# Performance work log

Measured on AMD Instinct MI355X. Metric: run time of the kernel, lower is better.

Reference implementation:

```python
import jax, jax.numpy as jnp
import numpy as np

T = S = 1024
B = 8
HID = 1024
H = 16
D = HID // H          # head_size = 64
RELK = 16             # max relative position (clip window)
NEG = -1e9


def setup_inputs() -> dict:
    key = jax.random.key(0)
    ks = jax.random.split(key, 12)
    inv = 1.0 / np.sqrt(HID)
    inp = {
        'q': jax.random.normal(ks[0], (T, B, HID), jnp.float32),
        'k': jax.random.normal(ks[1], (S, B, HID), jnp.float32),
        'v': jax.random.normal(ks[2], (S, B, HID), jnp.float32),
        # additive float mask (B,T,S): causal, masked positions = -1e9
        'mask': jnp.broadcast_to(jnp.triu(jnp.full((T, S), NEG, jnp.float32), k=1), (B, T, S)),
        'Wq': jax.random.normal(ks[3], (HID, HID), jnp.float32) * inv,
        'bq': jnp.zeros((HID,), jnp.float32),
        'Wk': jax.random.normal(ks[4], (HID, HID), jnp.float32) * inv,
        'bk': jnp.zeros((HID,), jnp.float32),
        'Wv': jax.random.normal(ks[5], (HID, HID), jnp.float32) * inv,
        'bv': jnp.zeros((HID,), jnp.float32),
        'Wo': jax.random.normal(ks[6], (HID, HID), jnp.float32) * inv,
        'bo': jnp.zeros((HID,), jnp.float32),
        'rel_k_table': jax.random.normal(ks[7], (2 * RELK + 1, D), jnp.float32) * 0.02,
        'rel_v_table': jax.random.normal(ks[8], (2 * RELK + 1, D), jnp.float32) * 0.02,
    }
    return inp


def _rel_index(t, s):
    # clipped relative position index (t, s) -> [0, 2*RELK]
    return jnp.clip(jnp.arange(s)[None, :] - jnp.arange(t)[:, None], -RELK, RELK) + RELK


def reference(q, k, v, mask, Wq, bq, Wk, bk, Wv, bv, Wo, bo, rel_k_table, rel_v_table):
    t, b, _ = q.shape
    scaling = D ** -0.5
    # projections; torch Linear: x @ W^T + b, here weights stored (in,out)
    qh = ((q @ Wq + bq) * scaling).reshape(t, b * H, D).transpose(1, 0, 2)  # (BH,T,D)
    kh = (k @ Wk + bk).reshape(-1, b * H, D).transpose(1, 0, 2)            # (BH,S,D)
    vh = (v @ Wv + bv).reshape(-1, b * H, D).transpose(1, 0, 2)            # (BH,S,D)
    s = kh.shape[1]

    score = jnp.einsum('ntd,nsd->nts', qh, kh)                 # (BH,T,S)
    idx = _rel_index(t, s)
    rel_k = rel_k_table[idx]                                   # (T,S,D)
    score = score + jnp.einsum('ntd,tsd->nts', qh, rel_k)      # relative-pos bias on scores

    score = (score.reshape(b, H, t, s) + mask[:, None]).reshape(b * H, t, s)
    attn = jax.nn.softmax(score, axis=-1)                      # dropout=0 (eval)

    o = jnp.einsum('nts,nsd->ntd', attn, vh)                   # (BH,T,D)
    rel_v = rel_v_table[idx]                                   # (T,S,D)
    o = o + jnp.einsum('nts,tsd->ntd', attn, rel_v)            # relative-pos bias on values

    o = o.transpose(1, 0, 2).reshape(t, b, H * D)              # (T,B,hidden)
    return o @ Wo + bo
```

## Files before the change

### kernel.cpp

```cpp
#include <hip/hip_runtime.h>

typedef unsigned short u16;
typedef __bf16 bf16x8 __attribute__((ext_vector_type(8)));
typedef __bf16 bf16x4v __attribute__((ext_vector_type(4)));
typedef short s16x4 __attribute__((ext_vector_type(4)));
typedef unsigned short u16x8 __attribute__((ext_vector_type(8)));
typedef unsigned short u16x4 __attribute__((ext_vector_type(4)));
typedef float f32x4 __attribute__((ext_vector_type(4)));


__device__ __forceinline__ u16 f2bf(float f) {
  return __builtin_bit_cast(u16, (__bf16)f);
}
__device__ __forceinline__ u16x8 pack_trunc8(float4 a, float4 b) {
  u16x8 t;
  t[0] = (u16)(__float_as_uint(a.x) >> 16); t[1] = (u16)(__float_as_uint(a.y) >> 16);
  t[2] = (u16)(__float_as_uint(a.z) >> 16); t[3] = (u16)(__float_as_uint(a.w) >> 16);
  t[4] = (u16)(__float_as_uint(b.x) >> 16); t[5] = (u16)(__float_as_uint(b.y) >> 16);
  t[6] = (u16)(__float_as_uint(b.z) >> 16); t[7] = (u16)(__float_as_uint(b.w) >> 16);
  return t;
}
__device__ __forceinline__ void barrier_lgkm() {
  __asm__ volatile("s_waitcnt lgkmcnt(0)\ns_barrier" ::: "memory");
}
typedef const __attribute__((address_space(1))) void* gas_ptr;
typedef __attribute__((address_space(3))) void* las_ptr;
__device__ __forceinline__ void load_lds16(const void* g, void* l) {
  __builtin_amdgcn_global_load_lds((gas_ptr)g, (las_ptr)l, 16, 0, 0);
}
__device__ __forceinline__ f32x4 mfma16(u16x4 a, u16x4 b, f32x4 c) {
#if __has_builtin(__builtin_amdgcn_mfma_f32_16x16x16_bf16)
  return __builtin_amdgcn_mfma_f32_16x16x16_bf16(
      __builtin_bit_cast(bf16x4v, a), __builtin_bit_cast(bf16x4v, b), c, 0, 0, 0);
#elif __has_builtin(__builtin_amdgcn_mfma_f32_16x16x16bf16_1k)
  return __builtin_amdgcn_mfma_f32_16x16x16bf16_1k(
      __builtin_bit_cast(s16x4, a), __builtin_bit_cast(s16x4, b), c, 0, 0, 0);
#else
  f32x4 d;
  __asm__ volatile("v_mfma_f32_16x16x16_bf16 %0, %1, %2, %3"
                   : "=v"(d) : "v"(a), "v"(b), "v"(c));
  return d;
#endif
}

__device__ __forceinline__ void transpose_body(const float* in, u16* out) {
  __shared__ u16 tile[64][65];
  const int r0 = blockIdx.y * 64, c0 = blockIdx.x * 64;
  const int tid = threadIdx.x;
  const int tr = tid >> 4, tc4 = (tid & 15) * 4;
#pragma unroll
  for (int p = 0; p < 4; ++p) {
    int r = tr + p * 16;
    float4 vv = *(const float4*)&in[(size_t)(r0 + r) * 1024 + c0 + tc4];
    tile[r][tc4 + 0] = f2bf(vv.x); tile[r][tc4 + 1] = f2bf(vv.y);
    tile[r][tc4 + 2] = f2bf(vv.z); tile[r][tc4 + 3] = f2bf(vv.w);
  }
  __syncthreads();
#pragma unroll
  for (int p = 0; p < 4; ++p) {
    int rr = tr + p * 16;
    ushort4 ov;
    ov.x = tile[tc4 + 0][rr]; ov.y = tile[tc4 + 1][rr];
    ov.z = tile[tc4 + 2][rr]; ov.w = tile[tc4 + 3][rr];
    *(ushort4*)&out[(size_t)(c0 + rr) * 1024 + r0 + tc4] = ov;
  }
}
__global__ __launch_bounds__(256) void transpose_cvt3_kernel(
    const float* w0, const float* w1, const float* w2,
    u16* o0, u16* o1, u16* o2)
{
  const float* in = blockIdx.z == 0 ? w0 : (blockIdx.z == 1 ? w1 : w2);
  u16* out = blockIdx.z == 0 ? o0 : (blockIdx.z == 1 ? o1 : o2);
  transpose_body(in, out);
}
__global__ __launch_bounds__(256) void transpose_cvt_kernel(
    const float* in, u16* out) { transpose_body(in, out); }

__global__ __launch_bounds__(256) void cvt3_kernel(
    const float* __restrict__ a, const float* __restrict__ b,
    const float* __restrict__ c,
    u16* __restrict__ oa, u16* __restrict__ ob, u16* __restrict__ oc)
{
  const float* in = blockIdx.z == 0 ? a : (blockIdx.z == 1 ? b : c);
  u16* out = blockIdx.z == 0 ? oa : (blockIdx.z == 1 ? ob : oc);
  const int n8 = (8192 * 1024) / 8;
  for (int i = blockIdx.x * 256 + threadIdx.x; i < n8; i += gridDim.x * 256) {
    float4 x = ((const float4*)in)[i * 2];
    float4 y = ((const float4*)in)[i * 2 + 1];
    *(u16x8*)&out[(size_t)i * 8] = pack_trunc8(x, y);
  }
}

struct GemmArgs {
  const u16* A; const u16* BT; const float* bias; void* out;
  float scale; int mode;
};

__global__ __launch_bounds__(256, 3) void gemm_lds_kernel(GemmArgs g0, GemmArgs g1)
{
  __shared__ __align__(16) u16 smem[24576];
  const GemmArgs g = blockIdx.z ? g1 : g0;
  const u16* __restrict__ A = g.A;
  const u16* __restrict__ BT = g.BT;
  const int tid = threadIdx.x;
  const int wave = tid >> 6, lane = tid & 63;
  const int quad = lane >> 4, l16 = lane & 15;
  const int wave_m = wave >> 1, wave_n = wave & 1;
  const int m0 = blockIdx.x * 128, n0 = blockIdx.y * 128;

  const int crow = tid >> 2;
  const int cq = (((tid & 3) ^ ((tid >> 3) & 3))) * 8;
  const int qswr = (quad ^ ((l16 >> 1) & 3)) * 8;

  f32x4 acc[4][4] = {};

  auto STAGE = [&](int bo, int kb) {
    const size_t ka = (size_t)kb * 32 + cq;
    load_lds16(&A [(size_t)(m0 + crow)      * 1024 + ka], &smem[bo + tid * 8]);
    load_lds16(&A [(size_t)(m0 + 64 + crow) * 1024 + ka], &smem[bo + 2048 + tid * 8]);
    load_lds16(&BT[(size_t)(n0 + crow)      * 1024 + ka], &smem[bo + 4096 + tid * 8]);
    load_lds16(&BT[(size_t)(n0 + 64 + crow) * 1024 + ka], &smem[bo + 6144 + tid * 8]);
  };

  int b0 = 0, b1 = 8192, b2 = 16384;
  STAGE(b0, 0);
  STAGE(b1, 1);
  for (int kb = 0; kb < 32; ++kb) {
    if (kb < 31)
      __asm__ volatile("s_waitcnt vmcnt(4) lgkmcnt(0)\ns_barrier" ::: "memory");
    else
      __asm__ volatile("s_waitcnt vmcnt(0) lgkmcnt(0)\ns_barrier" ::: "memory");
    if (kb + 2 < 32) STAGE(b2, kb + 2);
    const u16* As = &smem[b0];
    const u16* Bs = &smem[b0 + 4096];
    bf16x8 af[4], bfr[4];
#pragma unroll
    for (int mt = 0; mt < 4; ++mt)
      af[mt] = *(const bf16x8*)&As[(wave_m * 64 + mt * 16 + l16) * 32 + qswr];
#pragma unroll
    for (int nt = 0; nt < 4; ++nt)
      bfr[nt] = *(const bf16x8*)&Bs[(wave_n * 64 + nt * 16 + l16) * 32 + qswr];
#pragma unroll
    for (int mt = 0; mt < 4; ++mt)
#pragma unroll
      for (int nt = 0; nt < 4; ++nt)
        acc[mt][nt] = __builtin_amdgcn_mfma_f32_16x16x32_bf16(af[mt], bfr[nt], acc[mt][nt], 0, 0, 0);
    int t = b0; b0 = b1; b1 = b2; b2 = t;
  }

  const float scale = g.scale;
  if (g.mode == 0) {
#pragma unroll
    for (int mt = 0; mt < 4; ++mt)
#pragma unroll
      for (int nt = 0; nt < 4; ++nt) {
        int nn = n0 + wave_n * 64 + nt * 16 + l16;
        float bval = g.bias[nn];
#pragma unroll
        for (int reg = 0; reg < 4; ++reg) {
          int mm = m0 + wave_m * 64 + mt * 16 + quad * 4 + reg;
          ((float*)g.out)[(size_t)mm * 1024 + nn] = (acc[mt][nt][reg] + bval) * scale;
        }
      }
  } else {
    __syncthreads();
    u16* Cs = smem;
#pragma unroll
    for (int mt = 0; mt < 4; ++mt)
#pragma unroll
      for (int nt = 0; nt < 4; ++nt) {
        int nnl = wave_n * 64 + nt * 16 + l16;
        float bval = g.bias[n0 + nnl];
#pragma unroll
        for (int reg = 0; reg < 4; ++reg) {
          int mml = wave_m * 64 + mt * 16 + quad * 4 + reg;
          Cs[mml * 136 + nnl] = f2bf((acc[mt][nt][reg] + bval) * scale);
        }
      }
    __syncthreads();
    u16* out = (u16*)g.out;
    if (g.mode == 1) {
      int row = tid >> 1, half = tid & 1;
      int mm = m0 + row;
      int tt = mm >> 3, bbv = mm & 7;
      int hh = (n0 >> 6) + half;
      u16* dst = &out[(((size_t)(bbv * 16 + hh)) * 1024 + tt) * 64];
#pragma unroll
      for (int i = 0; i < 8; ++i)
        *(u16x8*)&dst[i * 8] = *(const u16x8*)&Cs[row * 136 + half * 64 + i * 8];
    } else {
      int t0 = m0 >> 3;
#pragma unroll
      for (int rr = 0; rr < 4; ++rr) {
        int rid = tid * 4 + rr;
        int nnv = rid >> 3, bbv = rid & 7;
        int hh = (n0 + nnv) >> 6, dd = (n0 + nnv) & 63;
        u16* dst = &out[(((size_t)(bbv * 16 + hh)) * 64 + dd) * 1024 + t0];
        u16x8 w0, w1;
#pragma unroll
        for (int t = 0; t < 8; ++t) w0[t] = Cs[(t * 8 + bbv) * 136 + nnv];
#pragma unroll
        for (int t = 0; t < 8; ++t) w1[t] = Cs[((t + 8) * 8 + bbv) * 136 + nnv];
        *(u16x8*)&dst[0] = w0;
        *(u16x8*)&dst[8] = w1;
      }
    }
  }
}

__global__ __launch_bounds__(256, 4) void attn_kernel(
    const u16* __restrict__ qh, const u16* __restrict__ kh,
    const u16* __restrict__ vt, const float* __restrict__ relk,
    const float* __restrict__ relv, u16* __restrict__ octx)
{
  const int n = blockIdx.x;
  const int q0 = (15 - blockIdx.y) * 64;
  const int tid = threadIdx.x;
  const int wave = tid >> 6, lane = tid & 63;
  const int quad = lane >> 4, l16 = lane & 15;
  const int rowi = wave * 16 + l16;
  const int trow = q0 + rowi;
  const float LOG2E = 1.442695040888963f;

  __shared__ __align__(16) u16 Ks[64 * 72];
  __shared__ __align__(16) u16 Vs[64 * 72];
  __shared__ float qrelS[64 * 17];
  __shared__ float wvS[17 * 64];
  __shared__ float relvS[17 * 64];

  const int diag = q0 >> 6;
  const int ntiles = diag + 1;

  bf16x8 qf[2];
#pragma unroll
  for (int kc = 0; kc < 2; ++kc)
    qf[kc] = *(const bf16x8*)&qh[((size_t)n * 1024 + trow) * 64 + kc * 32 + quad * 8];

  const u16* __restrict__ khn = kh + (size_t)n * 1024 * 64;
  const u16* __restrict__ vtn = vt + (size_t)n * 64 * 1024;

  u16x8 kA[2], vA[2], kB[2], vB[2];
  auto LOADT = [&](int s0, u16x8 (&kr)[2], u16x8 (&vr)[2]) {
#pragma unroll
    for (int j = 0; j < 2; ++j) {
      int c = j * 256 + tid;
      kr[j] = *(const u16x8*)&khn[(size_t)(s0 + (c >> 3)) * 64 + (c & 7) * 8];
      vr[j] = *(const u16x8*)&vtn[(size_t)(c >> 3) * 1024 + s0 + (c & 7) * 8];
    }
  };
  LOADT(0, kA, vA);
  if (1 < ntiles) LOADT(64, kB, vB);

  for (int i = tid; i < 17 * 64; i += 256) { wvS[i] = relk[i]; relvS[i] = relv[i]; }
  __syncthreads();

  float qreg[16];
#pragma unroll
  for (int kc = 0; kc < 2; ++kc)
#pragma unroll
    for (int jj = 0; jj < 8; ++jj)
      qreg[kc * 8 + jj] = (float)qf[kc][jj];
  float qrel0 = 0.f;
  for (int r = 0; r <= 16; ++r) {
    float s = 0.f;
#pragma unroll
    for (int kc = 0; kc < 2; ++kc)
#pragma unroll
      for (int jj = 0; jj < 8; ++jj)
        s += qreg[kc * 8 + jj] * wvS[r * 64 + kc * 32 + quad * 8 + jj];
    s += __shfl_xor(s, 16);
    s += __shfl_xor(s, 32);
    float sv = (s - 8.f) * LOG2E;
    if (r == 0) qrel0 = sv;
    if (quad == 0) qrelS[rowi * 17 + r] = sv;
  }
  __syncthreads();
  for (int i = tid; i < 17 * 64; i += 256) wvS[i] = 0.f;
  __syncthreads();

  f32x4 oacc[4] = {};
  float lrow = 0.f;

  auto WRITET = [&](u16x8 (&kr)[2], u16x8 (&vr)[2]) {
#pragma unroll
    for (int j = 0; j < 2; ++j) {
      int c = j * 256 + tid;
      *(u16x8*)&Ks[(c >> 3) * 72 + (c & 7) * 8] = kr[j];
      int d = c >> 3, c7 = c & 7;
      int vbase = d * 72 + (c7 & 1) * 32 + (c7 >> 1) * 4;
      u16x8 vv = vr[j];
      u16x4 vlo = {vv[0], vv[1], vv[2], vv[3]};
      u16x4 vhi = {vv[4], vv[5], vv[6], vv[7]};
      *(u16x4*)&Vs[vbase]      = vlo;
      *(u16x4*)&Vs[vbase + 16] = vhi;
    }
  };

  auto COMPUTE = [&](int st) {
    const int s0 = st * 64;
    f32x4 sc[4];
#pragma unroll
    for (int j = 0; j < 4; ++j) {
      f32x4 c4 = {};
#pragma unroll
      for (int kc = 0; kc < 2; ++kc) {
        bf16x8 kf = *(const bf16x8*)&Ks[(j * 16 + l16) * 72 + kc * 32 + quad * 8];
        c4 = __builtin_amdgcn_mfma_f32_16x16x32_bf16(kf, qf[kc], c4, 0, 0, 0);
      }
      sc[j] = c4;
    }

    u16x4 pfrag[4];
    if (st < diag - 1) {
#pragma unroll
      for (int j = 0; j < 4; ++j) {
        u16x4 pk;
#pragma unroll
        for (int reg = 0; reg < 4; ++reg) {
          float pv = exp2f(fmaf(sc[j][reg], LOG2E, qrel0));
          lrow += pv;
          pk[reg] = f2bf(pv);
        }
        pfrag[j] = pk;
      }
    } else {
#pragma unroll
      for (int j = 0; j < 4; ++j) {
        u16x4 pk;
#pragma unroll
        for (int reg = 0; reg < 4; ++reg) {
          int sel = s0 + j * 16 + quad * 4 + reg;
          int dt = trow - sel;
          float pv = 0.f;
          if (dt >= 0) {
            int r = (dt < 16) ? (16 - dt) : 0;
            pv = exp2f(fmaf(sc[j][reg], LOG2E, qrelS[rowi * 17 + r]));
            if (dt < 16) wvS[rowi * 17 + (16 - dt)] = pv;
          }
          lrow += pv;
          pk[reg] = f2bf(pv);
        }
        pfrag[j] = pk;
      }
    }

#pragma unroll
    for (int nt = 0; nt < 4; ++nt) {
#pragma unroll
      for (int jp = 0; jp < 2; ++jp) {
        u16x8 vv = *(const u16x8*)&Vs[(nt * 16 + l16) * 72 + quad * 16 + jp * 8];
        u16x4 vlo = {vv[0], vv[1], vv[2], vv[3]};
        u16x4 vhi = {vv[4], vv[5], vv[6], vv[7]};
        oacc[nt] = mfma16(vlo, pfrag[jp * 2],     oacc[nt]);
        oacc[nt] = mfma16(vhi, pfrag[jp * 2 + 1], oacc[nt]);
      }
    }
  };

  for (int st = 0; st < ntiles; st += 2) {
    if (st) barrier_lgkm();
    WRITET(kA, vA);
    barrier_lgkm();
    if (st + 2 < ntiles) LOADT((st + 2) * 64, kA, vA);
    COMPUTE(st);
    if (st + 1 >= ntiles) break;
    barrier_lgkm();
    WRITET(kB, vB);
    barrier_lgkm();
    if (st + 3 < ntiles) LOADT((st + 3) * 64, kB, vB);
    COMPUTE(st + 1);
  }

  lrow += __shfl_xor(lrow, 16);
  lrow += __shfl_xor(lrow, 32);

  float wvr[17];
  float bsum = 0.f;
#pragma unroll
  for (int r = 1; r <= 16; ++r) { wvr[r] = wvS[rowi * 17 + r]; bsum += wvr[r]; }
  wvr[0] = lrow - bsum;
  float linv = 1.f / lrow;

  const int hh = n & 15, bb = n >> 4;
  size_t base = ((size_t)trow * 8 + bb) * 1024 + hh * 64;
#pragma unroll
  for (int nt = 0; nt < 4; ++nt) {
    u16x4 ov;
#pragma unroll
    for (int reg = 0; reg < 4; ++reg) {
      int d = nt * 16 + quad * 4 + reg;
      float rv = 0.f;
#pragma unroll
      for (int r = 0; r <= 16; ++r) rv += wvr[r] * relvS[r * 64 + d];
      ov[reg] = f2bf((oacc[nt][reg] + rv) * linv);
    }
    *(u16x4*)&octx[base + nt * 16 + quad * 4] = ov;
  }
}

extern "C" void kernel_launch(void* const* d_in, const int* in_sizes, int n_in,
                              void* d_out, int out_size, void* d_ws, size_t ws_size,
                              hipStream_t stream) {
  (void)in_sizes; (void)n_in; (void)out_size; (void)ws_size;
  const float* q    = (const float*)d_in[0];
  const float* k    = (const float*)d_in[1];
  const float* v    = (const float*)d_in[2];
  const float* Wq   = (const float*)d_in[4];
  const float* bq   = (const float*)d_in[5];
  const float* Wk   = (const float*)d_in[6];
  const float* bk   = (const float*)d_in[7];
  const float* Wv   = (const float*)d_in[8];
  const float* bv   = (const float*)d_in[9];
  const float* Wo   = (const float*)d_in[10];
  const float* bo   = (const float*)d_in[11];
  const float* relk = (const float*)d_in[12];
  const float* relv = (const float*)d_in[13];
  float* out = (float*)d_out;

  char* ws = (char*)d_ws;
  u16* vt   = (u16*)(ws);
  u16* qh   = (u16*)(ws + ((size_t)16 << 20));
  u16* kh   = (u16*)(ws + ((size_t)32 << 20));
  u16* vbf  = kh;
  u16* octx = (u16*)(ws + ((size_t)48 << 20));
  u16* wqt  = (u16*)(ws + ((size_t)48 << 20));
  u16* wkt  = (u16*)(ws + ((size_t)50 << 20));
  u16* wvt  = (u16*)(ws + ((size_t)52 << 20));
  u16* wot  = kh;
  u16* qbf  = (u16*)d_out;
  u16* kbf  = (u16*)d_out + ((size_t)8 << 20);

  dim3 blk(256);
  transpose_cvt3_kernel<<<dim3(16, 16, 3), blk, 0, stream>>>(Wq, Wk, Wv, wqt, wkt, wvt);

  cvt3_kernel<<<dim3(2048, 1, 3), blk, 0, stream>>>(q, k, v, qbf, kbf, vbf);

  GemmArgs gv{vbf, wvt, bv, vt, 1.0f, 2};
  gemm_lds_kernel<<<dim3(64, 8, 1), blk, 0, stream>>>(gv, gv);

  GemmArgs gq{qbf, wqt, bq, qh, 0.125f, 1};
  GemmArgs gk{kbf, wkt, bk, kh, 1.0f,   1};
  gemm_lds_kernel<<<dim3(64, 8, 2), blk, 0, stream>>>(gq, gk);

  attn_kernel<<<dim3(128, 16), blk, 0, stream>>>(qh, kh, vt, relk, relv, octx);

  transpose_cvt_kernel<<<dim3(16, 16), blk, 0, stream>>>(Wo, wot);

  GemmArgs go{octx, wot, bo, out, 1.0f, 0};
  gemm_lds_kernel<<<dim3(64, 8, 1), blk, 0, stream>>>(go, go);
}
```

Measured before the change: 339.3 us.

## Fuse fp32-to-bf16 input conversion into QKV projection GEMM and batch all three

Removes the separate cvt3 kernel that converted q/k/v from fp32 to bf16. The GEMM now loads fp32 A tiles into registers, truncates them to bf16, and writes them to LDS one stage ahead, with B still loaded directly into LDS. The Q, K and V projections run as one launch with grid z=3. This saves a full read and write of the bf16 copies plus two launches. In exchange, A traffic per tile doubles in bytes and the pipeline holds more registers and waits on a different vmcnt.

```diff
diff --git a/kernel.cpp b/kernel.cpp
--- a/kernel.cpp
+++ b/kernel.cpp
@@ -76,31 +76,16 @@
 __global__ __launch_bounds__(256) void transpose_cvt_kernel(
     const float* in, u16* out) { transpose_body(in, out); }
 
-__global__ __launch_bounds__(256) void cvt3_kernel(
-    const float* __restrict__ a, const float* __restrict__ b,
-    const float* __restrict__ c,
-    u16* __restrict__ oa, u16* __restrict__ ob, u16* __restrict__ oc)
-{
-  const float* in = blockIdx.z == 0 ? a : (blockIdx.z == 1 ? b : c);
-  u16* out = blockIdx.z == 0 ? oa : (blockIdx.z == 1 ? ob : oc);
-  const int n8 = (8192 * 1024) / 8;
-  for (int i = blockIdx.x * 256 + threadIdx.x; i < n8; i += gridDim.x * 256) {
-    float4 x = ((const float4*)in)[i * 2];
-    float4 y = ((const float4*)in)[i * 2 + 1];
-    *(u16x8*)&out[(size_t)i * 8] = pack_trunc8(x, y);
-  }
-}
-
 struct GemmArgs {
-  const u16* A; const u16* BT; const float* bias; void* out;
+  const void* A; const u16* BT; const float* bias; void* out;
   float scale; int mode;
 };
 
-__global__ __launch_bounds__(256, 3) void gemm_lds_kernel(GemmArgs g0, GemmArgs g1)
-{
+template <int AFP32>
+__device__ __forceinline__ void gemm_body(GemmArgs g) {
   __shared__ __align__(16) u16 smem[24576];
-  const GemmArgs g = blockIdx.z ? g1 : g0;
-  const u16* __restrict__ A = g.A;
+  const u16* __restrict__ A16 = (const u16*)g.A;
+  const float* __restrict__ A32 = (const float*)g.A;
   const u16* __restrict__ BT = g.BT;
   const int tid = threadIdx.x;
   const int wave = tid >> 6, lane = tid & 63;
@@ -113,24 +98,56 @@
   const int qswr = (quad ^ ((l16 >> 1) & 3)) * 8;
 
   f32x4 acc[4][4] = {};
-
-  auto STAGE = [&](int bo, int kb) {
+  float4 ar[4];
+
+  auto AREG_LOAD = [&](int kb) {
     const size_t ka = (size_t)kb * 32 + cq;
-    load_lds16(&A [(size_t)(m0 + crow)      * 1024 + ka], &smem[bo + tid * 8]);
-    load_lds16(&A [(size_t)(m0 + 64 + crow) * 1024 + ka], &smem[bo + 2048 + tid * 8]);
-    load_lds16(&BT[(size_t)(n0 + crow)      * 1024 + ka], &smem[bo + 4096 + tid * 8]);
+    const float* p0 = &A32[(size_t)(m0 + crow) * 1024 + ka];
+    const float* p1 = &A32[(size_t)(m0 + 64 + crow) * 1024 + ka];
+    ar[0] = *(const float4*)p0; ar[1] = *(const float4*)(p0 + 4);
+    ar[2] = *(const float4*)p1; ar[3] = *(const float4*)(p1 + 4);
+  };
+  auto DS_WRITE_A = [&](int bo) {
+    *(u16x8*)&smem[bo + tid * 8]        = pack_trunc8(ar[0], ar[1]);
+    *(u16x8*)&smem[bo + 2048 + tid * 8] = pack_trunc8(ar[2], ar[3]);
+  };
+  auto STAGE_BT = [&](int bo, int kb) {
+    const size_t ka = (size_t)kb * 32 + cq;
+    load_lds16(&BT[(size_t)(n0 + crow) * 1024 + ka],      &smem[bo + 4096 + tid * 8]);
     load_lds16(&BT[(size_t)(n0 + 64 + crow) * 1024 + ka], &smem[bo + 6144 + tid * 8]);
   };
+  auto STAGE_A16 = [&](int bo, int kb) {
+    const size_t ka = (size_t)kb * 32 + cq;
+    load_lds16(&A16[(size_t)(m0 + crow) * 1024 + ka],      &smem[bo + tid * 8]);
+    load_lds16(&A16[(size_t)(m0 + 64 + crow) * 1024 + ka], &smem[bo + 2048 + tid * 8]);
+  };
 
   int b0 = 0, b1 = 8192, b2 = 16384;
-  STAGE(b0, 0);
-  STAGE(b1, 1);
+  if (AFP32) {
+    AREG_LOAD(0);
+    STAGE_BT(b0, 0);
+    DS_WRITE_A(b0);
+    AREG_LOAD(1);
+    STAGE_BT(b1, 1);
+  } else {
+    STAGE_A16(b0, 0); STAGE_BT(b0, 0);
+    STAGE_A16(b1, 1); STAGE_BT(b1, 1);
+  }
   for (int kb = 0; kb < 32; ++kb) {
-    if (kb < 31)
-      __asm__ volatile("s_waitcnt vmcnt(4) lgkmcnt(0)\ns_barrier" ::: "memory");
-    else
+    if (kb < 31) {
+      if (AFP32)
+        __asm__ volatile("s_waitcnt vmcnt(6) lgkmcnt(0)\ns_barrier" ::: "memory");
+      else
+        __asm__ volatile("s_waitcnt vmcnt(4) lgkmcnt(0)\ns_barrier" ::: "memory");
+    } else {
       __asm__ volatile("s_waitcnt vmcnt(0) lgkmcnt(0)\ns_barrier" ::: "memory");
-    if (kb + 2 < 32) STAGE(b2, kb + 2);
+    }
+    if (AFP32) {
+      if (kb + 1 < 32) DS_WRITE_A(b1);
+      if (kb + 2 < 32) { AREG_LOAD(kb + 2); STAGE_BT(b2, kb + 2); }
+    } else {
+      if (kb + 2 < 32) { STAGE_A16(b2, kb + 2); STAGE_BT(b2, kb + 2); }
+    }
     const u16* As = &smem[b0];
     const u16* Bs = &smem[b0 + 4096];
     bf16x8 af[4], bfr[4];
@@ -206,6 +223,12 @@
       }
     }
   }
+}
+
+template <int AFP32>
+__global__ __launch_bounds__(256, 3) void gemm_kernel(GemmArgs g0, GemmArgs g1, GemmArgs g2)
+{
+  gemm_body<AFP32>(blockIdx.z == 0 ? g0 : (blockIdx.z == 1 ? g1 : g2));
 }
 
 __global__ __launch_bounds__(256, 4) void attn_kernel(
@@ -421,31 +444,24 @@
   u16* vt   = (u16*)(ws);
   u16* qh   = (u16*)(ws + ((size_t)16 << 20));
   u16* kh   = (u16*)(ws + ((size_t)32 << 20));
-  u16* vbf  = kh;
   u16* octx = (u16*)(ws + ((size_t)48 << 20));
   u16* wqt  = (u16*)(ws + ((size_t)48 << 20));
   u16* wkt  = (u16*)(ws + ((size_t)50 << 20));
   u16* wvt  = (u16*)(ws + ((size_t)52 << 20));
   u16* wot  = kh;
-  u16* qbf  = (u16*)d_out;
-  u16* kbf  = (u16*)d_out + ((size_t)8 << 20);
 
   dim3 blk(256);
   transpose_cvt3_kernel<<<dim3(16, 16, 3), blk, 0, stream>>>(Wq, Wk, Wv, wqt, wkt, wvt);
 
-  cvt3_kernel<<<dim3(2048, 1, 3), blk, 0, stream>>>(q, k, v, qbf, kbf, vbf);
-
-  GemmArgs gv{vbf, wvt, bv, vt, 1.0f, 2};
-  gemm_lds_kernel<<<dim3(64, 8, 1), blk, 0, stream>>>(gv, gv);
-
-  GemmArgs gq{qbf, wqt, bq, qh, 0.125f, 1};
-  GemmArgs gk{kbf, wkt, bk, kh, 1.0f,   1};
-  gemm_lds_kernel<<<dim3(64, 8, 2), blk, 0, stream>>>(gq, gk);
+  GemmArgs gq{q, wqt, bq, qh, 0.125f, 1};
+  GemmArgs gk{k, wkt, bk, kh, 1.0f,   1};
+  GemmArgs gv{v, wvt, bv, vt, 1.0f,   2};
+  gemm_kernel<1><<<dim3(64, 8, 3), blk, 0, stream>>>(gq, gk, gv);
 
   attn_kernel<<<dim3(128, 16), blk, 0, stream>>>(qh, kh, vt, relk, relv, octx);
 
   transpose_cvt_kernel<<<dim3(16, 16), blk, 0, stream>>>(Wo, wot);
 
   GemmArgs go{octx, wot, bo, out, 1.0f, 0};
-  gemm_lds_kernel<<<dim3(64, 8, 1), blk, 0, stream>>>(go, go);
-}
+  gemm_kernel<0><<<dim3(64, 8, 1), blk, 0, stream>>>(go, go, go);
+}
```

Result: no change. 335.8 us (-1.0%).
